# Performance work log

Measured on AMD Instinct MI355X. Metric: run time of the kernel, lower is better.

## Reference

```python
import jax, jax.numpy as jnp
import numpy as np

D = 768
B, T = 4, 4096


def _layernorm(x, gamma, bias):
    # Faithful to the (buggy) original: (x - mu/sqrt(var)) * gamma + bias,
    # with torch's default unbiased variance (ddof=1).
    mu = jnp.mean(x, axis=-1, keepdims=True)
    var = jnp.var(x, axis=-1, keepdims=True, ddof=1)
    return (x - mu / jnp.sqrt(var)) * gamma + bias


def setup_inputs() -> dict:
    key = jax.random.key(0)
    ks = jax.random.split(key, 8)
    # kaiming_uniform_ default: bound = sqrt(6 / fan_in) with a=sqrt(5) -> gain = sqrt(2/(1+5)) = sqrt(1/3)
    # bound = gain * sqrt(3/fan_in) = sqrt(1/fan_in)
    bound_attn = 1.0 / np.sqrt(D)
    bound_lin = 1.0 / np.sqrt(D)  # torch Linear default init bound
    return {
        "x": jax.random.normal(ks[0], (B, T, D), dtype=jnp.float32),
        "ln1_g": jnp.ones((D,), jnp.float32),
        "ln1_b": jnp.zeros((D,), jnp.float32),
        "wq": jax.random.uniform(ks[1], (D, D), jnp.float32, -bound_attn, bound_attn),
        "wk": jax.random.uniform(ks[2], (D, D), jnp.float32, -bound_attn, bound_attn),
        "wv": jax.random.uniform(ks[3], (D, D), jnp.float32, -bound_attn, bound_attn),
        "ln2_g": jnp.ones((D,), jnp.float32),
        "ln2_b": jnp.zeros((D,), jnp.float32),
        "fc1_w": jax.random.uniform(ks[4], (D, D), jnp.float32, -bound_lin, bound_lin),
        "fc1_b": jax.random.uniform(ks[5], (D,), jnp.float32, -bound_lin, bound_lin),
        "fc2_w": jax.random.uniform(ks[6], (D, D), jnp.float32, -bound_lin, bound_lin),
        "fc2_b": jax.random.uniform(ks[7], (D,), jnp.float32, -bound_lin, bound_lin),
    }


def reference(x, ln1_g, ln1_b, wq, wk, wv, ln2_g, ln2_b, fc1_w, fc1_b, fc2_w, fc2_b):
    d_model = x.shape[-1]
    # LN 1
    y = _layernorm(x, ln1_g, ln1_b)
    # Naive single-head attention (no causal mask, scale 1/sqrt(d_model))
    q = jnp.einsum("btk,kd->btd", y, wq)
    k = jnp.einsum("btk,kd->btd", y, wk)
    v = jnp.einsum("btk,kd->btd", y, wv)
    scale = 1.0 / jnp.sqrt(jnp.asarray(d_model, y.dtype))
    a = jax.nn.softmax(jnp.einsum("bqd,bkd->bqk", q, k) * scale, axis=-1)
    y = jnp.einsum("bqt,btd->bqd", a, v)
    # LN 2
    y = _layernorm(y, ln2_g, ln2_b)
    # MLP: Linear -> ReLU -> Linear (Dropout in eval mode = identity)
    h = jax.nn.relu(jnp.einsum("btd,od->bto", y, fc1_w) + fc1_b)
    y = jnp.einsum("btd,od->bto", h, fc2_w) + fc2_b
    # Residual
    return x + y
```

## Files before the change

### kernel.cpp

```cpp
#include <hip/hip_runtime.h>
#include <hip/hip_bf16.h>


#define DDIM 768
#define TT   4096
#define NB   4
#define ROWS (NB * TT)

using bf16 = __hip_bfloat16;
typedef __bf16 bf16x8 __attribute__((ext_vector_type(8)));
typedef float  f32x4  __attribute__((ext_vector_type(4)));

__device__ __forceinline__ float to_f(float x) { return x; }
__device__ __forceinline__ float to_f(bf16 x) { return __bfloat162float(x); }

__device__ __forceinline__ void gload16(const void* g, void* l) {
#if __has_builtin(__builtin_amdgcn_global_load_lds)
  __builtin_amdgcn_global_load_lds(
      (const __attribute__((address_space(1))) void*)g,
      (__attribute__((address_space(3))) void*)l, 16, 0, 0);
#else
  int lane = threadIdx.x & 63;
  ((int4*)l)[lane] = *(const int4*)g;
#endif
}

template <int MODE, int NT, int MT>
__global__ __launch_bounds__(256) void gemm_bt(
    const bf16* __restrict__ A, int lda, long sA,
    const bf16* __restrict__ B, int ldb, long sB,
    void* __restrict__ Cout, int ldc, long sC, int K, float scale,
    const float* __restrict__ bias, const float* __restrict__ resid,
    float* __restrict__ Lsum) {
  __shared__ __align__(16) bf16 As[128 * 32];
  __shared__ __align__(16) bf16 Bs[128 * 32];
  __shared__ float Lred[128];

  int bx, by, bz;
  if constexpr (NT > 0) {
    const int h   = blockIdx.x;
    const int xcd = h & 7;
    const int s   = h >> 3;
    bx = s % NT;
    const int group = (s / NT) * 8 + xcd;
    by = group % MT;
    bz = group / MT;
  } else {
    bx = blockIdx.x; by = blockIdx.y; bz = blockIdx.z;
  }

  A += (long)bz * sA;
  B += (long)bz * sB;

  const int tid  = threadIdx.x;
  const int wave = tid >> 6;
  const int lane = tid & 63;
  const int l16  = lane & 15;
  const int lq   = lane >> 4;
  const int wm   = wave >> 1;
  const int wn   = wave & 1;
  const long tileM = (long)by * 128;
  const long tileN = (long)bx * 128;

  if constexpr (MODE == 5) {
    if (tid < 128) Lred[tid] = 0.f;
  }

  f32x4 acc[4][4] = {};

  const int c0 = wave * 128 + lane;
  const int c1 = c0 + 64;
  bf16* ldsA0 = &As[(wave * 128 + 0) * 8];
  bf16* ldsA1 = &As[(wave * 128 + 64) * 8];
  bf16* ldsB0 = &Bs[(wave * 128 + 0) * 8];
  bf16* ldsB1 = &Bs[(wave * 128 + 64) * 8];
  const long ar0 = (tileM + (c0 >> 2)) * (long)lda + (c0 & 3) * 8;
  const long ar1 = (tileM + (c1 >> 2)) * (long)lda + (c1 & 3) * 8;
  const long br0 = (tileN + (c0 >> 2)) * (long)ldb + (c0 & 3) * 8;
  const long br1 = (tileN + (c1 >> 2)) * (long)ldb + (c1 & 3) * 8;

  for (int k0 = 0; k0 < K; k0 += 32) {
    gload16(A + ar0 + k0, ldsA0);
    gload16(A + ar1 + k0, ldsA1);
    gload16(B + br0 + k0, ldsB0);
    gload16(B + br1 + k0, ldsB1);
    __syncthreads();

    bf16x8 af[4], bf_[4];
#pragma unroll
    for (int i = 0; i < 4; ++i)
      af[i] = *(const bf16x8*)&As[(wm * 64 + i * 16 + l16) * 32 + lq * 8];
#pragma unroll
    for (int j = 0; j < 4; ++j)
      bf_[j] = *(const bf16x8*)&Bs[(wn * 64 + j * 16 + l16) * 32 + lq * 8];
#pragma unroll
    for (int i = 0; i < 4; ++i)
#pragma unroll
      for (int j = 0; j < 4; ++j)
        acc[i][j] = __builtin_amdgcn_mfma_f32_16x16x32_bf16(af[i], bf_[j],
                                                            acc[i][j], 0, 0, 0);
    __syncthreads();
  }

  char* Cz = (char*)Cout;
  const long base_m = tileM + wm * 64;
  const long base_n = tileN + wn * 64;

  if constexpr (MODE == 5) {
    float ps[4][4] = {};
#pragma unroll
    for (int i = 0; i < 4; ++i)
#pragma unroll
      for (int j = 0; j < 4; ++j)
#pragma unroll
        for (int r = 0; r < 4; ++r) {
          const long row = base_m + i * 16 + lq * 4 + r;
          const long col = base_n + j * 16 + l16;
          float p = __expf(acc[i][j][r] * scale);
          ((bf16*)Cz)[(long)bz * sC + row * ldc + col] = __float2bfloat16(p);
          ps[i][r] += p;
        }
#pragma unroll
    for (int i = 0; i < 4; ++i)
#pragma unroll
      for (int r = 0; r < 4; ++r) {
        float v = ps[i][r];
        v += __shfl_xor(v, 1);
        v += __shfl_xor(v, 2);
        v += __shfl_xor(v, 4);
        v += __shfl_xor(v, 8);
        if (l16 == 0)
          atomicAdd(&Lred[wm * 64 + i * 16 + lq * 4 + r], v);
      }
    __syncthreads();
    if (tid < 128) atomicAdd(&Lsum[(long)bz * TT + tileM + tid], Lred[tid]);
  } else if constexpr (MODE == 6) {
#pragma unroll
    for (int i = 0; i < 4; ++i)
#pragma unroll
      for (int r = 0; r < 4; ++r) {
        const long row = base_m + i * 16 + lq * 4 + r;
        const float inv = 1.0f / Lsum[(long)bz * TT + row];
#pragma unroll
        for (int j = 0; j < 4; ++j) {
          const long col = base_n + j * 16 + l16;
          ((bf16*)Cz)[(long)bz * sC + row * ldc + col] =
              __float2bfloat16(acc[i][j][r] * inv);
        }
      }
  } else {
#pragma unroll
    for (int i = 0; i < 4; ++i)
#pragma unroll
      for (int j = 0; j < 4; ++j)
#pragma unroll
        for (int r = 0; r < 4; ++r) {
          const long row = base_m + i * 16 + lq * 4 + r;
          const long col = base_n + j * 16 + l16;
          float v = acc[i][j][r];
          if constexpr (MODE == 3) {
            v += bias[col];
            v = v > 0.f ? v : 0.f;
            ((bf16*)Cz)[(long)bz * sC + row * ldc + col] = __float2bfloat16(v);
          } else {
            v += bias[col] + resid[row * ldc + col];
            ((float*)Cz)[(long)bz * sC + row * ldc + col] = v;
          }
        }
  }
}

__global__ __launch_bounds__(256) void gemm_qkv(
    const bf16* __restrict__ A,
    const bf16* __restrict__ Wq, const bf16* __restrict__ Wk,
    const bf16* __restrict__ Wv, bf16* __restrict__ Qm,
    bf16* __restrict__ Km, bf16* __restrict__ Vt) {
  __shared__ __align__(16) bf16 As[128 * 32];
  __shared__ __align__(16) bf16 Bs[128 * 32];

  const int z = blockIdx.z;
  const bf16* B = (z == 0) ? Wq : (z == 1) ? Wk : Wv;

  const int tid  = threadIdx.x;
  const int wave = tid >> 6;
  const int lane = tid & 63;
  const int l16  = lane & 15;
  const int lq   = lane >> 4;
  const int wm   = wave >> 1;
  const int wn   = wave & 1;
  const long tileM = (long)blockIdx.y * 128;
  const long tileN = (long)blockIdx.x * 128;

  f32x4 acc[4][4] = {};

  const int c0 = wave * 128 + lane;
  const int c1 = c0 + 64;
  bf16* ldsA0 = &As[(wave * 128 + 0) * 8];
  bf16* ldsA1 = &As[(wave * 128 + 64) * 8];
  bf16* ldsB0 = &Bs[(wave * 128 + 0) * 8];
  bf16* ldsB1 = &Bs[(wave * 128 + 64) * 8];
  const long ar0 = (tileM + (c0 >> 2)) * (long)DDIM + (c0 & 3) * 8;
  const long ar1 = (tileM + (c1 >> 2)) * (long)DDIM + (c1 & 3) * 8;
  const long br0 = (tileN + (c0 >> 2)) * (long)DDIM + (c0 & 3) * 8;
  const long br1 = (tileN + (c1 >> 2)) * (long)DDIM + (c1 & 3) * 8;

  for (int k0 = 0; k0 < DDIM; k0 += 32) {
    gload16(A + ar0 + k0, ldsA0);
    gload16(A + ar1 + k0, ldsA1);
    gload16(B + br0 + k0, ldsB0);
    gload16(B + br1 + k0, ldsB1);
    __syncthreads();

    bf16x8 af[4], bf_[4];
#pragma unroll
    for (int i = 0; i < 4; ++i)
      af[i] = *(const bf16x8*)&As[(wm * 64 + i * 16 + l16) * 32 + lq * 8];
#pragma unroll
    for (int j = 0; j < 4; ++j)
      bf_[j] = *(const bf16x8*)&Bs[(wn * 64 + j * 16 + l16) * 32 + lq * 8];
#pragma unroll
    for (int i = 0; i < 4; ++i)
#pragma unroll
      for (int j = 0; j < 4; ++j)
        acc[i][j] = __builtin_amdgcn_mfma_f32_16x16x32_bf16(af[i], bf_[j],
                                                            acc[i][j], 0, 0, 0);
    __syncthreads();
  }

  const long base_m = tileM + wm * 64;
  const long base_n = tileN + wn * 64;
  bf16* Cp = (z == 0) ? Qm : (z == 1) ? Km : Vt;
#pragma unroll
  for (int i = 0; i < 4; ++i) {
#pragma unroll
    for (int j = 0; j < 4; ++j) {
#pragma unroll
      for (int r = 0; r < 4; ++r) {
        const long row = base_m + i * 16 + lq * 4 + r;
        const long col = base_n + j * 16 + l16;
        float v = acc[i][j][r];
        if (z < 2)
          Cp[row * DDIM + col] = __float2bfloat16(v);
        else
          Cp[col * (long)ROWS + row] = __float2bfloat16(v);
      }
    }
  }
}

template <typename T>
__global__ __launch_bounds__(256) void ln_kernel(
    const T* __restrict__ in, const float* __restrict__ g,
    const float* __restrict__ beta, bf16* __restrict__ out,
    float* __restrict__ Lzero) {
  const long row = blockIdx.x;
  if (Lzero != nullptr && threadIdx.x == 0) Lzero[row] = 0.f;
  const T* xr = in + row * DDIM;
  const int t = threadIdx.x;
  float v0 = to_f(xr[t]), v1 = to_f(xr[t + 256]), v2 = to_f(xr[t + 512]);
  float s = v0 + v1 + v2;
  float q = v0 * v0 + v1 * v1 + v2 * v2;
#pragma unroll
  for (int o = 32; o; o >>= 1) {
    s += __shfl_down(s, o);
    q += __shfl_down(q, o);
  }
  __shared__ float sb[4], qb[4];
  if ((t & 63) == 0) { sb[t >> 6] = s; qb[t >> 6] = q; }
  __syncthreads();
  const float S = sb[0] + sb[1] + sb[2] + sb[3];
  const float Q = qb[0] + qb[1] + qb[2] + qb[3];
  const float mu  = S * (1.0f / 768.0f);
  const float var = (Q - 768.0f * mu * mu) * (1.0f / 767.0f);
  const float sub = mu / sqrtf(var);
  bf16* orow = out + row * DDIM;
  orow[t]       = __float2bfloat16((v0 - sub) * g[t]       + beta[t]);
  orow[t + 256] = __float2bfloat16((v1 - sub) * g[t + 256] + beta[t + 256]);
  orow[t + 512] = __float2bfloat16((v2 - sub) * g[t + 512] + beta[t + 512]);
}

__global__ void prep_weights(const float* __restrict__ wq,
                             const float* __restrict__ wk,
                             const float* __restrict__ wv,
                             const float* __restrict__ f1,
                             const float* __restrict__ f2,
                             bf16* wqt, bf16* wkt, bf16* wvt, bf16* f1b,
                             bf16* f2b) {
  __shared__ float tile[32][33];
  const float* src;
  bf16* dst;
  bool tr = true;
  switch (blockIdx.z) {
    case 0: src = wq; dst = wqt; break;
    case 1: src = wk; dst = wkt; break;
    case 2: src = wv; dst = wvt; break;
    case 3: src = f1; dst = f1b; tr = false; break;
    default: src = f2; dst = f2b; tr = false; break;
  }
  const int tx = threadIdx.x, ty = threadIdx.y;
  const int x = blockIdx.x * 32 + tx;
  const int y = blockIdx.y * 32 + ty;
  if (tr) {
#pragma unroll
    for (int r = 0; r < 4; ++r) tile[ty + 8 * r][tx] = src[(y + 8 * r) * DDIM + x];
    __syncthreads();
    const int ox = blockIdx.y * 32 + tx;
    const int oy = blockIdx.x * 32 + ty;
#pragma unroll
    for (int r = 0; r < 4; ++r)
      dst[(oy + 8 * r) * DDIM + ox] = __float2bfloat16(tile[tx][ty + 8 * r]);
  } else {
#pragma unroll
    for (int r = 0; r < 4; ++r)
      dst[(y + 8 * r) * DDIM + x] = __float2bfloat16(src[(y + 8 * r) * DDIM + x]);
  }
}

extern "C" void kernel_launch(void* const* d_in, const int* in_sizes, int n_in,
                              void* d_out, int out_size, void* d_ws,
                              size_t ws_size, hipStream_t stream) {
  const float* x     = (const float*)d_in[0];
  const float* ln1_g = (const float*)d_in[1];
  const float* ln1_b = (const float*)d_in[2];
  const float* wq    = (const float*)d_in[3];
  const float* wk    = (const float*)d_in[4];
  const float* wv    = (const float*)d_in[5];
  const float* ln2_g = (const float*)d_in[6];
  const float* ln2_b = (const float*)d_in[7];
  const float* f1w   = (const float*)d_in[8];
  const float* f1bias= (const float*)d_in[9];
  const float* f2w   = (const float*)d_in[10];
  const float* f2bias= (const float*)d_in[11];
  float* out = (float*)d_out;

  char* ws = (char*)d_ws;
  size_t off = 0;
  auto take = [&](size_t bytes) -> char* {
    char* p = ws + off;
    off += (bytes + 255) & ~(size_t)255;
    return p;
  };
  const size_t WB = (size_t)DDIM * DDIM * sizeof(bf16);
  const size_t MB = (size_t)ROWS * DDIM * sizeof(bf16);
  bf16* wqt = (bf16*)take(WB);
  bf16* wkt = (bf16*)take(WB);
  bf16* wvt = (bf16*)take(WB);
  bf16* f1b = (bf16*)take(WB);
  bf16* f2b = (bf16*)take(WB);
  float* Lsum = (float*)take((size_t)ROWS * sizeof(float));
  bf16* y1  = (bf16*)take(MB);
  bf16* Qm  = (bf16*)take(MB);
  bf16* Km  = (bf16*)take(MB);
  bf16* Vt  = (bf16*)take(MB);
  bf16* Sb  = (bf16*)take((size_t)NB * TT * TT * sizeof(bf16));
  bf16* O  = y1;
  bf16* y2 = Qm;
  bf16* h  = Km;

  prep_weights<<<dim3(24, 24, 5), dim3(32, 8), 0, stream>>>(
      wq, wk, wv, f1w, f2w, wqt, wkt, wvt, f1b, f2b);

  ln_kernel<float><<<ROWS, 256, 0, stream>>>(x, ln1_g, ln1_b, y1, Lsum);

  gemm_qkv<<<dim3(6, 128, 3), 256, 0, stream>>>(y1, wqt, wkt, wvt, Qm, Km, Vt);

  const float scale = 0.03608439182435161f;
  gemm_bt<5, 32, 32><<<dim3(32 * 32 * NB), 256, 0, stream>>>(
      Qm, DDIM, (long)TT * DDIM, Km, DDIM, (long)TT * DDIM, Sb, TT,
      (long)TT * TT, DDIM, scale, nullptr, nullptr, Lsum);

  gemm_bt<6, 6, 32><<<dim3(6 * 32 * NB), 256, 0, stream>>>(
      Sb, TT, (long)TT * TT, Vt, ROWS, (long)TT, O, DDIM, (long)TT * DDIM, TT,
      1.f, nullptr, nullptr, Lsum);

  ln_kernel<bf16><<<ROWS, 256, 0, stream>>>(O, ln2_g, ln2_b, y2, nullptr);

  gemm_bt<3, 0, 0><<<dim3(6, 128, 1), 256, 0, stream>>>(
      y2, DDIM, 0, f1b, DDIM, 0, h, DDIM, 0, DDIM, 1.f, f1bias, nullptr,
      nullptr);
  gemm_bt<4, 0, 0><<<dim3(6, 128, 1), 256, 0, stream>>>(
      h, DDIM, 0, f2b, DDIM, 0, out, DDIM, 0, DDIM, 1.f, f2bias, x, nullptr);
}
```

Before: 632.3 us.

## Store attention probabilities and V in FP8 and use FP8 MFMA for PV

The unnormalized softmax probabilities and the transposed V matrix are now written as FP8 e4m3 instead of bf16. A new PV kernel consumes them with fp8 MFMA instructions, which halves the bytes of the large score matrix written and read. Epilogues for the QK, QKV and fc1 GEMMs are also staged through an LDS tile so global stores are coalesced vectors rather than scattered scalar writes. The cost is reduced precision in the attention weights and V, which the output tolerance may or may not absorb.

```diff
diff --git a/kernel.cpp b/kernel.cpp
--- a/kernel.cpp
+++ b/kernel.cpp
@@ -1,11 +1,13 @@
 #include <hip/hip_runtime.h>
 #include <hip/hip_bf16.h>
+#include <hip/hip_fp8.h>
 
 
 #define DDIM 768
 #define TT   4096
 #define NB   4
 #define ROWS (NB * TT)
+#define CTS  136
 
 using bf16 = __hip_bfloat16;
 typedef __bf16 bf16x8 __attribute__((ext_vector_type(8)));
@@ -13,6 +15,11 @@
 
 __device__ __forceinline__ float to_f(float x) { return x; }
 __device__ __forceinline__ float to_f(bf16 x) { return __bfloat162float(x); }
+
+__device__ __forceinline__ unsigned char to_fp8(float f) {
+  __hip_fp8_e4m3 t(f);
+  return (unsigned char)t.__x;
+}
 
 __device__ __forceinline__ void gload16(const void* g, void* l) {
 #if __has_builtin(__builtin_amdgcn_global_load_lds)
@@ -32,9 +39,11 @@
     void* __restrict__ Cout, int ldc, long sC, int K, float scale,
     const float* __restrict__ bias, const float* __restrict__ resid,
     float* __restrict__ Lsum) {
-  __shared__ __align__(16) bf16 As[128 * 32];
-  __shared__ __align__(16) bf16 Bs[128 * 32];
+  constexpr int SMEMN = (MODE == 4) ? 8192 : (128 * CTS);
+  __shared__ __align__(16) bf16 smem[SMEMN];
   __shared__ float Lred[128];
+  bf16* As = smem;
+  bf16* Bs = smem + 4096;
 
   int bx, by, bz;
   if constexpr (NT > 0) {
@@ -102,11 +111,8 @@
     __syncthreads();
   }
 
-  char* Cz = (char*)Cout;
-  const long base_m = tileM + wm * 64;
-  const long base_n = tileN + wn * 64;
-
   if constexpr (MODE == 5) {
+    bf16* ctile = smem;
     float ps[4][4] = {};
 #pragma unroll
     for (int i = 0; i < 4; ++i)
@@ -114,10 +120,9 @@
       for (int j = 0; j < 4; ++j)
 #pragma unroll
         for (int r = 0; r < 4; ++r) {
-          const long row = base_m + i * 16 + lq * 4 + r;
-          const long col = base_n + j * 16 + l16;
           float p = __expf(acc[i][j][r] * scale);
-          ((bf16*)Cz)[(long)bz * sC + row * ldc + col] = __float2bfloat16(p);
+          ctile[(wm * 64 + i * 16 + lq * 4 + r) * CTS + wn * 64 + j * 16 + l16] =
+              __float2bfloat16(p);
           ps[i][r] += p;
         }
 #pragma unroll
@@ -129,25 +134,45 @@
         v += __shfl_xor(v, 2);
         v += __shfl_xor(v, 4);
         v += __shfl_xor(v, 8);
-        if (l16 == 0)
-          atomicAdd(&Lred[wm * 64 + i * 16 + lq * 4 + r], v);
+        if (l16 == 0) atomicAdd(&Lred[wm * 64 + i * 16 + lq * 4 + r], v);
       }
     __syncthreads();
     if (tid < 128) atomicAdd(&Lsum[(long)bz * TT + tileM + tid], Lred[tid]);
-  } else if constexpr (MODE == 6) {
-#pragma unroll
-    for (int i = 0; i < 4; ++i)
-#pragma unroll
-      for (int r = 0; r < 4; ++r) {
-        const long row = base_m + i * 16 + lq * 4 + r;
-        const float inv = 1.0f / Lsum[(long)bz * TT + row];
-#pragma unroll
-        for (int j = 0; j < 4; ++j) {
-          const long col = base_n + j * 16 + l16;
-          ((bf16*)Cz)[(long)bz * sC + row * ldc + col] =
-              __float2bfloat16(acc[i][j][r] * inv);
+    unsigned char* Pz = (unsigned char*)Cout + (long)bz * sC;
+#pragma unroll
+    for (int p = 0; p < 8; ++p) {
+      const int rr = p * 16 + (tid >> 4);
+      const int cc = (tid & 15) * 8;
+      bf16x8 v = *(bf16x8*)&ctile[rr * CTS + cc];
+      union { unsigned char b[8]; uint2 u; } pk;
+#pragma unroll
+      for (int e = 0; e < 8; ++e) pk.b[e] = to_fp8((float)v[e]);
+      *(uint2*)&Pz[(long)(tileM + rr) * ldc + tileN + cc] = pk.u;
+    }
+  } else if constexpr (MODE == 3) {
+    bf16* ctile = smem;
+#pragma unroll
+    for (int j = 0; j < 4; ++j) {
+      const float bj = bias[tileN + wn * 64 + j * 16 + l16];
+#pragma unroll
+      for (int i = 0; i < 4; ++i)
+#pragma unroll
+        for (int r = 0; r < 4; ++r) {
+          float v = acc[i][j][r] + bj;
+          v = v > 0.f ? v : 0.f;
+          ctile[(wm * 64 + i * 16 + lq * 4 + r) * CTS + wn * 64 + j * 16 + l16] =
+              __float2bfloat16(v);
         }
-      }
+    }
+    __syncthreads();
+    bf16* Cb = (bf16*)Cout;
+#pragma unroll
+    for (int p = 0; p < 8; ++p) {
+      const int rr = p * 16 + (tid >> 4);
+      const int cc = (tid & 15) * 8;
+      float4 v = *(float4*)&ctile[rr * CTS + cc];
+      *(float4*)&Cb[(long)(tileM + rr) * ldc + tileN + cc] = v;
+    }
   } else {
 #pragma unroll
     for (int i = 0; i < 4; ++i)
@@ -155,18 +180,96 @@
       for (int j = 0; j < 4; ++j)
 #pragma unroll
         for (int r = 0; r < 4; ++r) {
-          const long row = base_m + i * 16 + lq * 4 + r;
-          const long col = base_n + j * 16 + l16;
-          float v = acc[i][j][r];
-          if constexpr (MODE == 3) {
-            v += bias[col];
-            v = v > 0.f ? v : 0.f;
-            ((bf16*)Cz)[(long)bz * sC + row * ldc + col] = __float2bfloat16(v);
-          } else {
-            v += bias[col] + resid[row * ldc + col];
-            ((float*)Cz)[(long)bz * sC + row * ldc + col] = v;
-          }
+          const long row = tileM + wm * 64 + i * 16 + lq * 4 + r;
+          const long col = tileN + wn * 64 + j * 16 + l16;
+          float v = acc[i][j][r] + bias[col] + resid[row * ldc + col];
+          ((float*)Cout)[row * ldc + col] = v;
         }
+  }
+}
+
+__global__ __launch_bounds__(256) void gemm_pv(
+    const unsigned char* __restrict__ P,
+    const unsigned char* __restrict__ Vt,
+    bf16* __restrict__ O,
+    const float* __restrict__ Lsum) {
+  __shared__ __align__(16) unsigned char smem8[128 * CTS * 2];
+  unsigned char* As8 = smem8;
+  unsigned char* Bs8 = smem8 + 4096;
+  bf16* ctile = (bf16*)smem8;
+
+  const int h   = blockIdx.x;
+  const int xcd = h & 7;
+  const int s   = h >> 3;
+  const int bx  = s % 6;
+  const int grp = (s / 6) * 8 + xcd;
+  const int by  = grp % 32;
+  const int bz  = grp / 32;
+
+  const int tid  = threadIdx.x;
+  const int wave = tid >> 6;
+  const int lane = tid & 63;
+  const int l16  = lane & 15;
+  const int lq   = lane >> 4;
+  const int wm   = wave >> 1;
+  const int wn   = wave & 1;
+  const long tileM = (long)by * 128;
+  const long tileN = (long)bx * 128;
+
+  const unsigned char* Pz = P + (long)bz * TT * TT;
+  const unsigned char* Vz = Vt + (long)bz * TT;
+
+  f32x4 acc[4][4] = {};
+
+  const int c = wave * 64 + lane;
+  const long pa = (tileM + (c >> 1)) * (long)TT + (c & 1) * 16;
+  const long va = (tileN + (c >> 1)) * (long)ROWS + (c & 1) * 16;
+  unsigned char* ldsA = As8 + wave * 1024;
+  unsigned char* ldsB = Bs8 + wave * 1024;
+
+  for (int k0 = 0; k0 < TT; k0 += 32) {
+    gload16(Pz + pa + k0, ldsA);
+    gload16(Vz + va + k0, ldsB);
+    __syncthreads();
+
+    long af[4], bfr[4];
+#pragma unroll
+    for (int i = 0; i < 4; ++i)
+      af[i] = *(const long*)&As8[(wm * 64 + i * 16 + l16) * 32 + lq * 8];
+#pragma unroll
+    for (int j = 0; j < 4; ++j)
+      bfr[j] = *(const long*)&Bs8[(wn * 64 + j * 16 + l16) * 32 + lq * 8];
+#pragma unroll
+    for (int i = 0; i < 4; ++i)
+#pragma unroll
+      for (int j = 0; j < 4; ++j)
+        acc[i][j] = __builtin_amdgcn_mfma_f32_16x16x32_fp8_fp8(
+            af[i], bfr[j], acc[i][j], 0, 0, 0);
+    __syncthreads();
+  }
+
+  float inv[4][4];
+#pragma unroll
+  for (int i = 0; i < 4; ++i)
+#pragma unroll
+    for (int r = 0; r < 4; ++r)
+      inv[i][r] =
+          1.0f / Lsum[(long)bz * TT + tileM + wm * 64 + i * 16 + lq * 4 + r];
+#pragma unroll
+  for (int i = 0; i < 4; ++i)
+#pragma unroll
+    for (int j = 0; j < 4; ++j)
+#pragma unroll
+      for (int r = 0; r < 4; ++r)
+        ctile[(wm * 64 + i * 16 + lq * 4 + r) * CTS + wn * 64 + j * 16 + l16] =
+            __float2bfloat16(acc[i][j][r] * inv[i][r]);
+  __syncthreads();
+#pragma unroll
+  for (int p = 0; p < 8; ++p) {
+    const int rr = p * 16 + (tid >> 4);
+    const int cc = (tid & 15) * 8;
+    float4 v = *(float4*)&ctile[rr * CTS + cc];
+    *(float4*)&O[((long)bz * TT + tileM + rr) * DDIM + tileN + cc] = v;
   }
 }
 
@@ -174,9 +277,11 @@
     const bf16* __restrict__ A,
     const bf16* __restrict__ Wq, const bf16* __restrict__ Wk,
     const bf16* __restrict__ Wv, bf16* __restrict__ Qm,
-    bf16* __restrict__ Km, bf16* __restrict__ Vt) {
-  __shared__ __align__(16) bf16 As[128 * 32];
-  __shared__ __align__(16) bf16 Bs[128 * 32];
+    bf16* __restrict__ Km, unsigned char* __restrict__ Vt) {
+  __shared__ __align__(16) bf16 smem[128 * CTS];
+  bf16* As = smem;
+  bf16* Bs = smem + 4096;
+  bf16* ctile = smem;
 
   const int z = blockIdx.z;
   const bf16* B = (z == 0) ? Wq : (z == 1) ? Wk : Wv;
@@ -227,23 +332,45 @@
     __syncthreads();
   }
 
-  const long base_m = tileM + wm * 64;
-  const long base_n = tileN + wn * 64;
-  bf16* Cp = (z == 0) ? Qm : (z == 1) ? Km : Vt;
-#pragma unroll
-  for (int i = 0; i < 4; ++i) {
-#pragma unroll
-    for (int j = 0; j < 4; ++j) {
-#pragma unroll
-      for (int r = 0; r < 4; ++r) {
-        const long row = base_m + i * 16 + lq * 4 + r;
-        const long col = base_n + j * 16 + l16;
-        float v = acc[i][j][r];
-        if (z < 2)
-          Cp[row * DDIM + col] = __float2bfloat16(v);
-        else
-          Cp[col * (long)ROWS + row] = __float2bfloat16(v);
+  if (z < 2) {
+#pragma unroll
+    for (int i = 0; i < 4; ++i)
+#pragma unroll
+      for (int j = 0; j < 4; ++j)
+#pragma unroll
+        for (int r = 0; r < 4; ++r)
+          ctile[(wm * 64 + i * 16 + lq * 4 + r) * CTS + wn * 64 + j * 16 + l16] =
+              __float2bfloat16(acc[i][j][r]);
+    __syncthreads();
+    bf16* Cp = (z == 0) ? Qm : Km;
+#pragma unroll
+    for (int p = 0; p < 8; ++p) {
+      const int rr = p * 16 + (tid >> 4);
+      const int cc = (tid & 15) * 8;
+      float4 v = *(float4*)&ctile[rr * CTS + cc];
+      *(float4*)&Cp[(long)(tileM + rr) * DDIM + tileN + cc] = v;
+    }
+  } else {
+#pragma unroll
+    for (int i = 0; i < 4; ++i)
+#pragma unroll
+      for (int j = 0; j < 4; ++j) {
+        union { bf16 h[4]; uint2 u; } w;
+#pragma unroll
+        for (int r = 0; r < 4; ++r) w.h[r] = __float2bfloat16(acc[i][j][r]);
+        *(uint2*)&ctile[(wn * 64 + j * 16 + l16) * CTS + wm * 64 + i * 16 +
+                        lq * 4] = w.u;
       }
+    __syncthreads();
+#pragma unroll
+    for (int p = 0; p < 8; ++p) {
+      const int rr = p * 16 + (tid >> 4);
+      const int cc = (tid & 15) * 8;
+      bf16x8 v = *(bf16x8*)&ctile[rr * CTS + cc];
+      union { unsigned char b[8]; uint2 u; } pk;
+#pragma unroll
+      for (int e = 0; e < 8; ++e) pk.b[e] = to_fp8((float)v[e]);
+      *(uint2*)&Vt[(long)(tileN + rr) * ROWS + tileM + cc] = pk.u;
     }
   }
 }
@@ -351,8 +478,8 @@
   bf16* y1  = (bf16*)take(MB);
   bf16* Qm  = (bf16*)take(MB);
   bf16* Km  = (bf16*)take(MB);
-  bf16* Vt  = (bf16*)take(MB);
-  bf16* Sb  = (bf16*)take((size_t)NB * TT * TT * sizeof(bf16));
+  unsigned char* Vt8 = (unsigned char*)take((size_t)DDIM * ROWS);
+  unsigned char* Sb8 = (unsigned char*)take((size_t)NB * TT * TT);
   bf16* O  = y1;
   bf16* y2 = Qm;
   bf16* h  = Km;
@@ -362,16 +489,14 @@
 
   ln_kernel<float><<<ROWS, 256, 0, stream>>>(x, ln1_g, ln1_b, y1, Lsum);
 
-  gemm_qkv<<<dim3(6, 128, 3), 256, 0, stream>>>(y1, wqt, wkt, wvt, Qm, Km, Vt);
+  gemm_qkv<<<dim3(6, 128, 3), 256, 0, stream>>>(y1, wqt, wkt, wvt, Qm, Km, Vt8);
 
   const float scale = 0.03608439182435161f;
   gemm_bt<5, 32, 32><<<dim3(32 * 32 * NB), 256, 0, stream>>>(
-      Qm, DDIM, (long)TT * DDIM, Km, DDIM, (long)TT * DDIM, Sb, TT,
+      Qm, DDIM, (long)TT * DDIM, Km, DDIM, (long)TT * DDIM, Sb8, TT,
       (long)TT * TT, DDIM, scale, nullptr, nullptr, Lsum);
 
-  gemm_bt<6, 6, 32><<<dim3(6 * 32 * NB), 256, 0, stream>>>(
-      Sb, TT, (long)TT * TT, Vt, ROWS, (long)TT, O, DDIM, (long)TT * DDIM, TT,
-      1.f, nullptr, nullptr, Lsum);
+  gemm_pv<<<dim3(6 * 32 * NB), 256, 0, stream>>>(Sb8, Vt8, O, Lsum);
 
   ln_kernel<bf16><<<ROWS, 256, 0, stream>>>(O, ln2_g, ln2_b, y2, nullptr);
 
```

After: 647.4 us. +2.4%, slower.
